# Kernel optimization log

Measured on AMD Instinct MI355X. Metric: run time of the kernel, lower is better.

The kernel has to match this reference:

```python
import jax, jax.numpy as jnp
import numpy as np

CHUNK = 512

def setup_inputs() -> dict:
    key = jax.random.key(0)
    kq, kk, kv = jax.random.split(key, 3)
    shape = (1, 16, 8192, 64)  # B, H, N, E
    return {
        "query": jax.random.normal(kq, shape, dtype=jnp.float32),
        "key": jax.random.normal(kk, shape, dtype=jnp.float32),
        "value": jax.random.normal(kv, shape, dtype=jnp.float32),
    }

def reference(query, key, value):
    c = CHUNK
    B, H, N, E = query.shape
    nc = N // c  # number of query chunks (N assumed divisible by c)
    scale = 1.0 / (E ** 0.5)
    neg_inf = jnp.finfo(query.dtype).min

    qc = query.reshape(B, H, nc, c, E)
    kc = key.reshape(B, H, nc, c, E)
    vc = value.reshape(B, H, nc, c, E)

    # ---- chunk 0: window is just keys[0:c], standard causal mask ----
    s0 = jnp.einsum('bhqe,bhse->bhqs', qc[:, :, 0], kc[:, :, 0]) * scale
    mask0 = jnp.triu(jnp.ones((c, c), dtype=bool), k=1)
    a0 = jax.nn.softmax(jnp.where(mask0, neg_inf, s0), axis=-1)  # (B,H,c,c)
    o0 = jnp.einsum('bhqs,bhse->bhqe', a0, vc[:, :, 0])           # (B,H,c,E)

    # ---- chunks 1..nc-1: key window = [previous chunk, current chunk] ----
    kw = jnp.concatenate([kc[:, :, :-1], kc[:, :, 1:]], axis=3)  # (B,H,nc-1,2c,E)
    vw = jnp.concatenate([vc[:, :, :-1], vc[:, :, 1:]], axis=3)
    s = jnp.einsum('bhnqe,bhnse->bhnqs', qc[:, :, 1:], kw) * scale  # (B,H,nc-1,c,2c)
    # faithful to torch.triu(ones(q_len, k_len), diagonal=1): row r keeps cols 0..r
    mask = jnp.triu(jnp.ones((c, 2 * c), dtype=bool), k=1)
    a = jax.nn.softmax(jnp.where(mask, neg_inf, s), axis=-1)        # (B,H,nc-1,c,2c)
    o = jnp.einsum('bhnqs,bhnse->bhnqe', a, vw)                     # (B,H,nc-1,c,E)

    output = jnp.concatenate([o0, o.reshape(B, H, (nc - 1) * c, E)], axis=2)  # (B,H,N,E)
    # weights concatenated along the key axis (torch cat dim=3)
    a_rest = jnp.moveaxis(a, 2, 3).reshape(B, H, c, (nc - 1) * 2 * c)
    weights = jnp.concatenate([a0, a_rest], axis=3)  # (B,H,c, c + (nc-1)*2c)
    return output, weights
```

## Files before the change

kernel.cpp:

```cpp
#include <hip/hip_runtime.h>

typedef __bf16 bf16x8 __attribute__((ext_vector_type(8)));
typedef float  f32x4  __attribute__((ext_vector_type(4)));

#define NH    16
#define SEQ   8192
#define EDIM  64
#define CHK   512
#define WCOLS 15872
#define OUT0  8388608

#define MFMA(a, b, c) __builtin_amdgcn_mfma_f32_16x16x32_bf16((a), (b), (c), 0, 0, 0)

__global__ __launch_bounds__(512, 2) void chunked_attn_kernel(
    const float* __restrict__ Qg, const float* __restrict__ Kg,
    const float* __restrict__ Vg, float* __restrict__ out)
{
    __shared__ __align__(16) __bf16 lds_k[32768];
    __shared__ __align__(16) __bf16 lds_v[32768];
    __shared__ __align__(16) __bf16 lds_p[8][640];

    const int tid  = threadIdx.x;
    const int lane = tid & 63;
    const int wv   = tid >> 6;
    const int l16  = lane & 15;
    const int quad = lane >> 4;

    const int h  = blockIdx.x >> 4;
    const int n  = blockIdx.x & 15;
    const int ns = (n == 0) ? 0 : n - 1;

    const size_t qbase = ((size_t)h * SEQ + (size_t)n  * CHK) * EDIM;
    const size_t kbase = ((size_t)h * SEQ + (size_t)ns * CHK) * EDIM;
    float* __restrict__ W = out + OUT0;
    const size_t wrow0  = (size_t)h * CHK;
    const int    colbase = (n == 0) ? 0 : (CHK + (n - 1) * 2 * CHK);

    if (n != 0) {
        const size_t z0 = wrow0 * WCOLS + (size_t)(colbase + CHK);
        #pragma unroll 4
        for (int idx = tid; idx < 512 * 128; idx += 512) {
            const int r = idx >> 7, j = idx & 127;
            f32x4 z = {0.f, 0.f, 0.f, 0.f};
            __builtin_nontemporal_store(z, (f32x4*)(W + z0 + (size_t)r * WCOLS + (size_t)(j * 4)));
        }
    }

    #pragma unroll
    for (int it = 0; it < 8; ++it) {
        const int c = tid + it * 512;
        const int s = c >> 3, sub = c & 7;
        const float* src = Kg + kbase + (size_t)s * EDIM + sub * 8;
        const float4 a = *(const float4*)src;
        const float4 b = *(const float4*)(src + 4);
        bf16x8 t;
        t[0] = (__bf16)a.x; t[1] = (__bf16)a.y; t[2] = (__bf16)a.z; t[3] = (__bf16)a.w;
        t[4] = (__bf16)b.x; t[5] = (__bf16)b.y; t[6] = (__bf16)b.z; t[7] = (__bf16)b.w;
        const int idx = ((s >> 4) * 8 + sub) * 16 + (s & 15);
        ((bf16x8*)lds_k)[idx] = t;
    }

    #pragma unroll
    for (int it = 0; it < 8; ++it) {
        const int c = tid + it * 512;
        const int e = c & 63, sb = c >> 6;
        bf16x8 t;
        #pragma unroll
        for (int j = 0; j < 8; ++j)
            t[j] = (__bf16)Vg[kbase + (size_t)(sb * 8 + j) * EDIM + e];
        const int idx = (((sb >> 2) * 4 + (e >> 4)) * 4 + (sb & 3)) * 16 + (e & 15);
        ((bf16x8*)lds_v)[idx] = t;
    }

    __syncthreads();

    const float SC = 0.125f * 1.44269504088896340736f;
    __bf16* const pb = lds_p[wv];
    const bf16x8* const kf = (const bf16x8*)lds_k;
    const bf16x8* const vf = (const bf16x8*)lds_v;

    for (int mt = 0; mt < 4; ++mt) {
        const int m0 = wv * 64 + mt * 16;
        const int rq = m0 + quad * 4;

        bf16x8 aq0, aq1;
        {
            const float* qp = Qg + qbase + (size_t)(m0 + l16) * EDIM + quad * 8;
            float4 a = *(const float4*)(qp);
            float4 b = *(const float4*)(qp + 4);
            aq0[0]=(__bf16)(a.x*SC); aq0[1]=(__bf16)(a.y*SC); aq0[2]=(__bf16)(a.z*SC); aq0[3]=(__bf16)(a.w*SC);
            aq0[4]=(__bf16)(b.x*SC); aq0[5]=(__bf16)(b.y*SC); aq0[6]=(__bf16)(b.z*SC); aq0[7]=(__bf16)(b.w*SC);
            a = *(const float4*)(qp + 32);
            b = *(const float4*)(qp + 36);
            aq1[0]=(__bf16)(a.x*SC); aq1[1]=(__bf16)(a.y*SC); aq1[2]=(__bf16)(a.z*SC); aq1[3]=(__bf16)(a.w*SC);
            aq1[4]=(__bf16)(b.x*SC); aq1[5]=(__bf16)(b.y*SC); aq1[6]=(__bf16)(b.z*SC); aq1[7]=(__bf16)(b.w*SC);
        }

        f32x4 st[32];
        #pragma unroll
        for (int t = 0; t < 32; ++t) {
            const int kb = t * 128 + quad * 16 + l16;
            f32x4 acc = {0.f, 0.f, 0.f, 0.f};
            acc = MFMA(aq0, kf[kb],      acc);
            acc = MFMA(aq1, kf[kb + 64], acc);
            const int col = t * 16 + l16;
            #pragma unroll
            for (int r = 0; r < 4; ++r)
                acc[r] = (col <= rq + r) ? acc[r] : -3.0e38f;
            st[t] = acc;
        }

        float mr[4];
        #pragma unroll
        for (int r = 0; r < 4; ++r) mr[r] = st[0][r];
        #pragma unroll
        for (int t = 1; t < 32; ++t) {
            #pragma unroll
            for (int r = 0; r < 4; ++r) mr[r] = fmaxf(mr[r], st[t][r]);
        }
        #pragma unroll
        for (int r = 0; r < 4; ++r) {
            #pragma unroll
            for (int off = 1; off < 16; off <<= 1)
                mr[r] = fmaxf(mr[r], __shfl_xor(mr[r], off));
        }

        float lr[4] = {0.f, 0.f, 0.f, 0.f};
        #pragma unroll
        for (int t = 0; t < 32; ++t) {
            #pragma unroll
            for (int r = 0; r < 4; ++r) {
                const float e = __builtin_amdgcn_exp2f(st[t][r] - mr[r]);
                st[t][r] = e;
                lr[r] += e;
            }
        }
        float ri[4];
        #pragma unroll
        for (int r = 0; r < 4; ++r) {
            #pragma unroll
            for (int off = 1; off < 16; off <<= 1)
                lr[r] += __shfl_xor(lr[r], off);
            ri[r] = __builtin_amdgcn_rcpf(lr[r]);
        }

        f32x4 o0 = {0,0,0,0}, o1 = {0,0,0,0}, o2 = {0,0,0,0}, o3 = {0,0,0,0};
        float* const wbase = W + (wrow0 + (size_t)(m0 + l16)) * WCOLS + colbase;
        #pragma unroll
        for (int pr = 0; pr < 16; ++pr) {
            #pragma unroll
            for (int tt = 0; tt < 2; ++tt) {
                const int t = pr * 2 + tt;
                #pragma unroll
                for (int r = 0; r < 4; ++r) {
                    const float p = st[t][r] * ri[r];
                    pb[(quad * 4 + r) * 40 + tt * 16 + l16] = (__bf16)p;
                }
            }
            const bf16x8 pa = *(const bf16x8*)(pb + l16 * 40 + quad * 8);
            {
                f32x4 w0, w1;
                w0[0]=(float)pa[0]; w0[1]=(float)pa[1]; w0[2]=(float)pa[2]; w0[3]=(float)pa[3];
                w1[0]=(float)pa[4]; w1[1]=(float)pa[5]; w1[2]=(float)pa[6]; w1[3]=(float)pa[7];
                float* wp = wbase + pr * 32 + quad * 8;
                __builtin_nontemporal_store(w0, (f32x4*)wp);
                __builtin_nontemporal_store(w1, (f32x4*)(wp + 4));
            }
            const int vb = pr * 256 + quad * 16 + l16;
            o0 = MFMA(pa, vf[vb      ], o0);
            o1 = MFMA(pa, vf[vb +  64], o1);
            o2 = MFMA(pa, vf[vb + 128], o2);
            o3 = MFMA(pa, vf[vb + 192], o3);
        }

        const size_t ob = qbase + (size_t)rq * EDIM + l16;
        #pragma unroll
        for (int r = 0; r < 4; ++r) {
            __builtin_nontemporal_store(o0[r], out + ob + (size_t)r * EDIM     );
            __builtin_nontemporal_store(o1[r], out + ob + (size_t)r * EDIM + 16);
            __builtin_nontemporal_store(o2[r], out + ob + (size_t)r * EDIM + 32);
            __builtin_nontemporal_store(o3[r], out + ob + (size_t)r * EDIM + 48);
        }
    }
}

extern "C" void kernel_launch(void* const* d_in, const int* in_sizes, int n_in,
                              void* d_out, int out_size, void* d_ws, size_t ws_size,
                              hipStream_t stream) {
    const float* Q = (const float*)d_in[0];
    const float* K = (const float*)d_in[1];
    const float* V = (const float*)d_in[2];
    float* out = (float*)d_out;
    chunked_attn_kernel<<<dim3(256), dim3(512), 0, stream>>>(Q, K, V, out);
}
```

Measured before the change: 657.1 us.

## Split masked-weights zero fill into separate kernel and store fp32 weights directly

Moves the zero-fill of the masked half of each weights window into a dedicated high-parallelism kernel launched before the attention kernel. Weights are now stored directly from the fp32 normalized probabilities in MFMA output layout rather than from bf16 values read back from LDS. This aims to spread the large zero-store traffic over many more blocks than the 256-block main grid and to take weight stores out of the PV loop. The cost is an extra launch, the two kernels running serialized, and narrower per-lane store patterns.

```diff
diff --git a/kernel.cpp b/kernel.cpp
--- a/kernel.cpp
+++ b/kernel.cpp
@@ -11,6 +11,23 @@
 #define OUT0  8388608
 
 #define MFMA(a, b, c) __builtin_amdgcn_mfma_f32_16x16x32_bf16((a), (b), (c), 0, 0, 0)
+
+__global__ __launch_bounds__(256) void zero_fill_kernel(float* __restrict__ W) {
+    const int gid = blockIdx.x * 256 + threadIdx.x;
+    #pragma unroll
+    for (int it = 0; it < 30; ++it) {
+        const int i     = gid + it * 524288;
+        const int j     = i & 127;
+        const int rowid = i >> 7;
+        const int r     = rowid & 511;
+        const int w     = rowid >> 9;
+        const int h     = w / 15;
+        const int n     = w - h * 15 + 1;
+        float* p = W + (size_t)(h * 512 + r) * WCOLS + (size_t)n * 1024 + j * 4;
+        f32x4 z = {0.f, 0.f, 0.f, 0.f};
+        __builtin_nontemporal_store(z, (f32x4*)p);
+    }
+}
 
 __global__ __launch_bounds__(512, 2) void chunked_attn_kernel(
     const float* __restrict__ Qg, const float* __restrict__ Kg,
@@ -35,16 +52,6 @@
     float* __restrict__ W = out + OUT0;
     const size_t wrow0  = (size_t)h * CHK;
     const int    colbase = (n == 0) ? 0 : (CHK + (n - 1) * 2 * CHK);
-
-    if (n != 0) {
-        const size_t z0 = wrow0 * WCOLS + (size_t)(colbase + CHK);
-        #pragma unroll 4
-        for (int idx = tid; idx < 512 * 128; idx += 512) {
-            const int r = idx >> 7, j = idx & 127;
-            f32x4 z = {0.f, 0.f, 0.f, 0.f};
-            __builtin_nontemporal_store(z, (f32x4*)(W + z0 + (size_t)r * WCOLS + (size_t)(j * 4)));
-        }
-    }
 
     #pragma unroll
     for (int it = 0; it < 8; ++it) {
@@ -144,8 +151,18 @@
             ri[r] = __builtin_amdgcn_rcpf(lr[r]);
         }
 
+        {
+            float* const wp0 = W + (wrow0 + (size_t)rq) * WCOLS + colbase + l16;
+            #pragma unroll
+            for (int t = 0; t < 32; ++t) {
+                #pragma unroll
+                for (int r = 0; r < 4; ++r)
+                    __builtin_nontemporal_store(st[t][r] * ri[r],
+                        wp0 + (size_t)r * WCOLS + t * 16);
+            }
+        }
+
         f32x4 o0 = {0,0,0,0}, o1 = {0,0,0,0}, o2 = {0,0,0,0}, o3 = {0,0,0,0};
-        float* const wbase = W + (wrow0 + (size_t)(m0 + l16)) * WCOLS + colbase;
         #pragma unroll
         for (int pr = 0; pr < 16; ++pr) {
             #pragma unroll
@@ -158,14 +175,6 @@
                 }
             }
             const bf16x8 pa = *(const bf16x8*)(pb + l16 * 40 + quad * 8);
-            {
-                f32x4 w0, w1;
-                w0[0]=(float)pa[0]; w0[1]=(float)pa[1]; w0[2]=(float)pa[2]; w0[3]=(float)pa[3];
-                w1[0]=(float)pa[4]; w1[1]=(float)pa[5]; w1[2]=(float)pa[6]; w1[3]=(float)pa[7];
-                float* wp = wbase + pr * 32 + quad * 8;
-                __builtin_nontemporal_store(w0, (f32x4*)wp);
-                __builtin_nontemporal_store(w1, (f32x4*)(wp + 4));
-            }
             const int vb = pr * 256 + quad * 16 + l16;
             o0 = MFMA(pa, vf[vb      ], o0);
             o1 = MFMA(pa, vf[vb +  64], o1);
@@ -191,5 +200,6 @@
     const float* K = (const float*)d_in[1];
     const float* V = (const float*)d_in[2];
     float* out = (float*)d_out;
+    zero_fill_kernel<<<dim3(2048), dim3(256), 0, stream>>>(out + OUT0);
     chunked_attn_kernel<<<dim3(256), dim3(512), 0, stream>>>(Q, K, V, out);
 }
```

Measured after the change: 632.6 us. 3.7% less time.
